# Performance work log

Measured on AMD Instinct MI355X. Metric: run time of the kernel, lower is better.

## Reference

```python
import jax, jax.numpy as jnp
import numpy as np

EPS = 0.001   # EPSILON2
T1 = 1.0
T2 = 100.0
DISC = 16     # number of discrete features
B, F, K1, K2 = 524288, 16, 16, 8


def _enforce(v):
    # Enforced autograd fn: forward = max(v, EPS), backward = identity (STE)
    return v + jax.lax.stop_gradient(jnp.maximum(v, EPS) - v)


def _soft_bin(cont, interval, i_min):
    """cont: [B,F]; interval: [F,K]; i_min: [F]. Vectorized over features/bins.
    Returns (STE one-hot out [B, F*K], kmeans_loss scalar)."""
    # bin centers = i_min + running cumsum of (enforced) gaps -> [F,K]
    centers = i_min[:, None] + jnp.cumsum(_enforce(interval), axis=1)
    d = (cont[:, :, None] - centers[None, :, :]) ** 2          # [B,F,K]
    s1 = jax.nn.softmax(-T1 * d, axis=-1)                      # kmeans softmax
    kmeans_loss = jnp.sum(jnp.mean(jnp.sum(d * s1, axis=-1), axis=0))
    s2 = jax.nn.softmax(-T2 * d, axis=-1)                      # sharp softmax
    oh = jax.nn.one_hot(jnp.argmax(s2, axis=-1), d.shape[-1], dtype=s2.dtype)
    out = s2 + jax.lax.stop_gradient(oh - s2)                  # STE one-hot
    return out.reshape(cont.shape[0], -1), kmeans_loss


def setup_inputs() -> dict:
    key = jax.random.key(0)
    k1, k2, k3 = jax.random.split(key, 3)
    x = jax.random.uniform(k1, (B, DISC + F), dtype=jnp.float32)
    interval = jax.random.uniform(k2, (F, K1), dtype=jnp.float32,
                                  minval=0.01, maxval=0.12)
    interval2 = jax.random.uniform(k3, (F, K2), dtype=jnp.float32,
                                   minval=0.02, maxval=0.2)
    i_min = jnp.zeros((F,), dtype=jnp.float32)
    return {"x": x, "interval": interval, "interval2": interval2, "i_min": i_min}


def reference(x, interval, interval2, i_min):
    x_disc, cont = x[:, :DISC], x[:, DISC:]
    out1, loss1 = _soft_bin(cont, interval, i_min)
    out2, loss2 = _soft_bin(cont, interval2, i_min)
    total_out = jnp.concatenate([x_disc, out1, out2], axis=1)  # [B, DISC+F*(K1+K2)]
    return total_out, loss1 + loss2
```

## Files before the change

### kernel.cpp

```cpp
#include <hip/hip_runtime.h>


constexpr int kB      = 524288;
constexpr int kF      = 16;
constexpr int kK1     = 16;
constexpr int kK2     = 8;
constexpr int kRowIn  = 32;
constexpr int kRowOut = 400;
constexpr float kEps  = 0.001f;
constexpr int kTPB    = 256;
constexpr int kGrid   = kB / kTPB;
constexpr int kC4     = kRowOut / 4;
constexpr int kXStride = 33;

template <int K>
__device__ __forceinline__ int soft_argmax_loss(const float* __restrict__ dd,
                                                double& lacc)
{
#pragma clang fp contract(off)
    float se = 0.f, sde = 0.f;
#pragma unroll
    for (int k = 0; k < K; ++k) {
        float e = __expf(-dd[k]);
        se += e; sde += dd[k] * e;
    }
    lacc += (double)(sde / se);

    float z[K];
#pragma unroll
    for (int k = 0; k < K; ++k) z[k] = -100.0f * dd[k];
    float m = z[0]; int kmax = 0;
#pragma unroll
    for (int k = 1; k < K; ++k) {
        if (z[k] > m) { m = z[k]; kmax = k; }
    }

    bool cand = false;
#pragma unroll
    for (int k = 0; k < K; ++k)
        cand |= (k < kmax) & (z[k] >= m - 2.4e-7f);
    if (cand) {
        float e2[K]; float ss = 0.f;
        for (int k = 0; k < K; ++k) { e2[k] = expf(z[k] - m); ss += e2[k]; }
        int km = 0; float pmax = e2[0] / ss;
        for (int k = 1; k < K; ++k) {
            float p = e2[k] / ss;
            if (p > pmax) { pmax = p; km = k; }
        }
        kmax = km;
    }
    return kmax;
}

__global__ __launch_bounds__(kTPB) void binlayer_main(
    const float* __restrict__ x,
    const float* __restrict__ interval,
    const float* __restrict__ interval2,
    const float* __restrict__ i_min,
    float* __restrict__ out,
    double* __restrict__ partial)
{
#pragma clang fp contract(off)
    __shared__ float sC1[kF][kK1];
    __shared__ float sC2[kF][kK2];
    __shared__ float sX[kTPB * kXStride];
    __shared__ unsigned char sIdx[kTPB * kF];
    __shared__ double sL[kTPB / 64];

    const int tid = threadIdx.x;

    if (tid < kF) {
        const float base = i_min[tid];
        float run = 0.f;
        for (int k = 0; k < kK1; ++k) {
            run += fmaxf(interval[tid * kK1 + k], kEps);
            sC1[tid][k] = base + run;
        }
        run = 0.f;
        for (int k = 0; k < kK2; ++k) {
            run += fmaxf(interval2[tid * kK2 + k], kEps);
            sC2[tid][k] = base + run;
        }
    }

    const long long rowBase = (long long)blockIdx.x * kTPB;

    const float4* __restrict__ xin4 = (const float4*)(x + rowBase * kRowIn);
#pragma unroll
    for (int i = 0; i < (kTPB * kRowIn / 4) / kTPB; ++i) {
        int flat = i * kTPB + tid;
        float4 v = xin4[flat];
        int r = flat >> 3, c4 = flat & 7;
        float* p = &sX[r * kXStride + c4 * 4];
        p[0] = v.x; p[1] = v.y; p[2] = v.z; p[3] = v.w;
    }
    __syncthreads();

    double lacc = 0.0;
    const float* __restrict__ myc = &sX[tid * kXStride + 16];

#pragma unroll 1
    for (int f = 0; f < kF; ++f) {
        const float c = myc[f];

        float dd1[kK1];
#pragma unroll
        for (int k = 0; k < kK1; ++k) { float t = c - sC1[f][k]; dd1[k] = t * t; }
        int k1 = soft_argmax_loss<kK1>(dd1, lacc);

        float dd2[kK2];
#pragma unroll
        for (int k = 0; k < kK2; ++k) { float t = c - sC2[f][k]; dd2[k] = t * t; }
        int k2 = soft_argmax_loss<kK2>(dd2, lacc);

        sIdx[tid * kF + f] = (unsigned char)(k1 | (k2 << 4));
    }

#pragma unroll
    for (int off = 32; off > 0; off >>= 1) lacc += __shfl_down(lacc, off);
    if ((tid & 63) == 0) sL[tid >> 6] = lacc;

    __syncthreads();

    if (tid == 0) partial[blockIdx.x] = sL[0] + sL[1] + sL[2] + sL[3];

    float4* __restrict__ o4 = (float4*)(out + rowBase * kRowOut);
#pragma unroll 1
    for (int i = 0; i < kC4; ++i) {
        unsigned idx = (unsigned)(i * kTPB + tid);
        unsigned r = idx / 100u;
        unsigned c = idx - r * 100u;
        float4 o;
        if (c < 4u) {
            const float* p = &sX[r * kXStride + c * 4u];
            o.x = p[0]; o.y = p[1]; o.z = p[2]; o.w = p[3];
        } else if (c < 68u) {
            unsigned u = c - 4u, f = u >> 2, q = (u & 3u) * 4u;
            unsigned k = sIdx[r * kF + f] & 15u;
            o.x = (k == q + 0u) ? 1.f : 0.f;
            o.y = (k == q + 1u) ? 1.f : 0.f;
            o.z = (k == q + 2u) ? 1.f : 0.f;
            o.w = (k == q + 3u) ? 1.f : 0.f;
        } else {
            unsigned u = c - 68u, f = u >> 1, q = (u & 1u) * 4u;
            unsigned k = (unsigned)(sIdx[r * kF + f]) >> 4;
            o.x = (k == q + 0u) ? 1.f : 0.f;
            o.y = (k == q + 1u) ? 1.f : 0.f;
            o.z = (k == q + 2u) ? 1.f : 0.f;
            o.w = (k == q + 3u) ? 1.f : 0.f;
        }
        o4[idx] = o;
    }
}

__global__ __launch_bounds__(256) void binlayer_finalize(
    const double* __restrict__ partial,
    float* __restrict__ out)
{
    __shared__ double sL[4];
    const int tid = threadIdx.x;
    double s = 0.0;
#pragma unroll
    for (int i = 0; i < kGrid / 256; ++i)
        s += partial[i * 256 + tid];
#pragma unroll
    for (int off = 32; off > 0; off >>= 1) s += __shfl_down(s, off);
    if ((tid & 63) == 0) sL[tid >> 6] = s;
    __syncthreads();
    if (tid == 0)
        out[(long long)kB * kRowOut] =
            (float)((sL[0] + sL[1] + sL[2] + sL[3]) * (1.0 / (double)kB));
}

extern "C" void kernel_launch(void* const* d_in, const int* in_sizes, int n_in,
                              void* d_out, int out_size, void* d_ws, size_t ws_size,
                              hipStream_t stream)
{
    const float* x    = (const float*)d_in[0];
    const float* itv1 = (const float*)d_in[1];
    const float* itv2 = (const float*)d_in[2];
    const float* imin = (const float*)d_in[3];
    float* out = (float*)d_out;
    double* partial = (double*)d_ws;

    binlayer_main<<<kGrid, kTPB, 0, stream>>>(x, itv1, itv2, imin, out, partial);
    binlayer_finalize<<<1, 256, 0, stream>>>(partial, out);
}
```

Measured before the change: 892.4 us.

## Make each wave own its rows to drop block barriers; use nontemporal output stores

Each 64-lane wave now loads, processes and writes only its own 64 rows, so the block-wide barriers after the input load and before the output phase become per-wave LDS waitcnts. When the workspace is large enough, partial loss sums are written per wave, which removes the last barrier, and the finalize kernel loops over a variable count. Output stores use nontemporal hints to limit cache pollution from the large write-only stream. One block barrier is added after the centers setup. The per-wave output writes are less contiguous across the block, and the finalize kernel reads four times as many partials.

```diff
diff --git a/kernel.cpp b/kernel.cpp
--- a/kernel.cpp
+++ b/kernel.cpp
@@ -12,6 +12,9 @@
 constexpr int kGrid   = kB / kTPB;
 constexpr int kC4     = kRowOut / 4;
 constexpr int kXStride = 33;
+constexpr int kWPB    = kTPB / 64;
+
+typedef float f32x4 __attribute__((ext_vector_type(4)));
 
 template <int K>
 __device__ __forceinline__ int soft_argmax_loss(const float* __restrict__ dd,
@@ -58,16 +61,19 @@
     const float* __restrict__ interval2,
     const float* __restrict__ i_min,
     float* __restrict__ out,
-    double* __restrict__ partial)
+    double* __restrict__ partial,
+    int perwave)
 {
 #pragma clang fp contract(off)
     __shared__ float sC1[kF][kK1];
     __shared__ float sC2[kF][kK2];
     __shared__ float sX[kTPB * kXStride];
     __shared__ unsigned char sIdx[kTPB * kF];
-    __shared__ double sL[kTPB / 64];
+    __shared__ double sL[kWPB];
 
     const int tid = threadIdx.x;
+    const int w   = tid >> 6;
+    const int l   = tid & 63;
 
     if (tid < kF) {
         const float base = i_min[tid];
@@ -82,19 +88,21 @@
             sC2[tid][k] = base + run;
         }
     }
+    __syncthreads();
 
     const long long rowBase = (long long)blockIdx.x * kTPB;
-
-    const float4* __restrict__ xin4 = (const float4*)(x + rowBase * kRowIn);
-#pragma unroll
-    for (int i = 0; i < (kTPB * kRowIn / 4) / kTPB; ++i) {
-        int flat = i * kTPB + tid;
-        float4 v = xin4[flat];
-        int r = flat >> 3, c4 = flat & 7;
+    const int R0 = w * 64;
+
+    const f32x4* __restrict__ xin4 = (const f32x4*)(x + (rowBase + R0) * kRowIn);
+#pragma unroll
+    for (int i = 0; i < 8; ++i) {
+        int flat = i * 64 + l;
+        f32x4 v = xin4[flat];
+        int r = R0 + (flat >> 3), c4 = flat & 7;
         float* p = &sX[r * kXStride + c4 * 4];
         p[0] = v.x; p[1] = v.y; p[2] = v.z; p[3] = v.w;
     }
-    __syncthreads();
+    asm volatile("s_waitcnt lgkmcnt(0)" ::: "memory");
 
     double lacc = 0.0;
     const float* __restrict__ myc = &sX[tid * kXStride + 16];
@@ -115,54 +123,58 @@
 
         sIdx[tid * kF + f] = (unsigned char)(k1 | (k2 << 4));
     }
+    asm volatile("s_waitcnt lgkmcnt(0)" ::: "memory");
 
 #pragma unroll
     for (int off = 32; off > 0; off >>= 1) lacc += __shfl_down(lacc, off);
-    if ((tid & 63) == 0) sL[tid >> 6] = lacc;
-
-    __syncthreads();
-
-    if (tid == 0) partial[blockIdx.x] = sL[0] + sL[1] + sL[2] + sL[3];
-
-    float4* __restrict__ o4 = (float4*)(out + rowBase * kRowOut);
+    if (perwave) {
+        if (l == 0) partial[(long long)blockIdx.x * kWPB + w] = lacc;
+    } else {
+        if (l == 0) sL[w] = lacc;
+        __syncthreads();
+        if (tid == 0) partial[blockIdx.x] = sL[0] + sL[1] + sL[2] + sL[3];
+    }
+
+    f32x4* __restrict__ o4 = (f32x4*)(out + (rowBase + R0) * kRowOut);
 #pragma unroll 1
     for (int i = 0; i < kC4; ++i) {
-        unsigned idx = (unsigned)(i * kTPB + tid);
+        unsigned idx = (unsigned)(i * 64 + l);
         unsigned r = idx / 100u;
         unsigned c = idx - r * 100u;
-        float4 o;
+        unsigned rr = (unsigned)R0 + r;
+        f32x4 o;
         if (c < 4u) {
-            const float* p = &sX[r * kXStride + c * 4u];
+            const float* p = &sX[rr * kXStride + c * 4u];
             o.x = p[0]; o.y = p[1]; o.z = p[2]; o.w = p[3];
         } else if (c < 68u) {
             unsigned u = c - 4u, f = u >> 2, q = (u & 3u) * 4u;
-            unsigned k = sIdx[r * kF + f] & 15u;
+            unsigned k = sIdx[rr * kF + f] & 15u;
             o.x = (k == q + 0u) ? 1.f : 0.f;
             o.y = (k == q + 1u) ? 1.f : 0.f;
             o.z = (k == q + 2u) ? 1.f : 0.f;
             o.w = (k == q + 3u) ? 1.f : 0.f;
         } else {
             unsigned u = c - 68u, f = u >> 1, q = (u & 1u) * 4u;
-            unsigned k = (unsigned)(sIdx[r * kF + f]) >> 4;
+            unsigned k = (unsigned)(sIdx[rr * kF + f]) >> 4;
             o.x = (k == q + 0u) ? 1.f : 0.f;
             o.y = (k == q + 1u) ? 1.f : 0.f;
             o.z = (k == q + 2u) ? 1.f : 0.f;
             o.w = (k == q + 3u) ? 1.f : 0.f;
         }
-        o4[idx] = o;
+        __builtin_nontemporal_store(o, &o4[idx]);
     }
 }
 
 __global__ __launch_bounds__(256) void binlayer_finalize(
     const double* __restrict__ partial,
-    float* __restrict__ out)
+    float* __restrict__ out,
+    int n)
 {
     __shared__ double sL[4];
     const int tid = threadIdx.x;
     double s = 0.0;
-#pragma unroll
-    for (int i = 0; i < kGrid / 256; ++i)
-        s += partial[i * 256 + tid];
+    for (int i = tid; i < n; i += 256)
+        s += partial[i];
 #pragma unroll
     for (int off = 32; off > 0; off >>= 1) s += __shfl_down(s, off);
     if ((tid & 63) == 0) sL[tid >> 6] = s;
@@ -183,6 +195,9 @@
     float* out = (float*)d_out;
     double* partial = (double*)d_ws;
 
-    binlayer_main<<<kGrid, kTPB, 0, stream>>>(x, itv1, itv2, imin, out, partial);
-    binlayer_finalize<<<1, 256, 0, stream>>>(partial, out);
-}
+    const int perwave = (ws_size >= (size_t)kGrid * kWPB * sizeof(double)) ? 1 : 0;
+    const int nPartial = perwave ? kGrid * kWPB : kGrid;
+
+    binlayer_main<<<kGrid, kTPB, 0, stream>>>(x, itv1, itv2, imin, out, partial, perwave);
+    binlayer_finalize<<<1, 256, 0, stream>>>(partial, out, nPartial);
+}
```

Result: slower. 911.5 us (+2.1%).

## Split fused kernel into compute-indices and expand-output kernels via workspace

Applied to the files above, without the earlier changes.

Splits the single fused kernel into two. The first computes the packed bin indices and per-warp loss partials directly from global memory, without staging x in shared memory. The second reads those indices and x and writes the 400-float output rows in a fully coalesced grid-strided pattern. The aim is to drop the large shared-memory footprint, raising occupancy, and to let the memory-bound output write run as its own streaming kernel. In exchange it adds an 8 MB index round trip through global memory and an extra launch, and the new path only runs if the workspace is large enough.

```diff
diff --git a/kernel.cpp b/kernel.cpp
--- a/kernel.cpp
+++ b/kernel.cpp
@@ -12,6 +12,14 @@
 constexpr int kGrid   = kB / kTPB;
 constexpr int kC4     = kRowOut / 4;
 constexpr int kXStride = 33;
+constexpr int kWPB    = kTPB / 64;
+
+constexpr size_t kIdxBytes = (size_t)kB * kF;
+constexpr size_t kPartOff  = kIdxBytes;
+constexpr size_t kWsNeed   = kIdxBytes + (size_t)kGrid * kWPB * sizeof(double);
+
+typedef float f32x4 __attribute__((ext_vector_type(4)));
+typedef unsigned long long u64x2 __attribute__((ext_vector_type(2)));
 
 template <int K>
 __device__ __forceinline__ int soft_argmax_loss(const float* __restrict__ dd,
@@ -50,6 +58,108 @@
         kmax = km;
     }
     return kmax;
+}
+
+__device__ __forceinline__ f32x4 onehot4(unsigned k, unsigned q)
+{
+    f32x4 o;
+    o.x = (k == q + 0u) ? 1.f : 0.f;
+    o.y = (k == q + 1u) ? 1.f : 0.f;
+    o.z = (k == q + 2u) ? 1.f : 0.f;
+    o.w = (k == q + 3u) ? 1.f : 0.f;
+    return o;
+}
+
+__global__ __launch_bounds__(kTPB) void bin_compute(
+    const float* __restrict__ x,
+    const float* __restrict__ interval,
+    const float* __restrict__ interval2,
+    const float* __restrict__ i_min,
+    unsigned long long* __restrict__ idxbuf,
+    double* __restrict__ partial)
+{
+#pragma clang fp contract(off)
+    __shared__ float sC1[kF][kK1];
+    __shared__ float sC2[kF][kK2];
+
+    const int tid = threadIdx.x;
+    const int w   = tid >> 6;
+    const int l   = tid & 63;
+
+    if (tid < kF) {
+        const float base = i_min[tid];
+        float run = 0.f;
+        for (int k = 0; k < kK1; ++k) {
+            run += fmaxf(interval[tid * kK1 + k], kEps);
+            sC1[tid][k] = base + run;
+        }
+        run = 0.f;
+        for (int k = 0; k < kK2; ++k) {
+            run += fmaxf(interval2[tid * kK2 + k], kEps);
+            sC2[tid][k] = base + run;
+        }
+    }
+    __syncthreads();
+
+    const long long row = (long long)blockIdx.x * kTPB + tid;
+    const float* __restrict__ xr = x + row * kRowIn + 16;
+
+    double lacc = 0.0;
+    unsigned long long lo = 0ull, hi = 0ull;
+
+#pragma unroll 1
+    for (int f = 0; f < kF; ++f) {
+        const float c = xr[f];
+
+        float dd1[kK1];
+#pragma unroll
+        for (int k = 0; k < kK1; ++k) { float t = c - sC1[f][k]; dd1[k] = t * t; }
+        int k1 = soft_argmax_loss<kK1>(dd1, lacc);
+
+        float dd2[kK2];
+#pragma unroll
+        for (int k = 0; k < kK2; ++k) { float t = c - sC2[f][k]; dd2[k] = t * t; }
+        int k2 = soft_argmax_loss<kK2>(dd2, lacc);
+
+        const unsigned long long byte = (unsigned long long)(k1 | (k2 << 4));
+        if (f < 8) lo |= byte << (8 * f);
+        else       hi |= byte << (8 * (f - 8));
+    }
+
+    u64x2 pk; pk.x = lo; pk.y = hi;
+    *reinterpret_cast<u64x2*>(&idxbuf[row * 2]) = pk;
+
+#pragma unroll
+    for (int off = 32; off > 0; off >>= 1) lacc += __shfl_down(lacc, off);
+    if (l == 0) partial[(long long)blockIdx.x * kWPB + w] = lacc;
+}
+
+__global__ __launch_bounds__(kTPB) void bin_expand(
+    const float* __restrict__ x,
+    const unsigned char* __restrict__ ib,
+    float* __restrict__ out)
+{
+    const unsigned t0 = blockIdx.x * kTPB + threadIdx.x;
+    f32x4* __restrict__ o4 = (f32x4*)out;
+
+#pragma unroll 1
+    for (int s = 0; s < kC4; ++s) {
+        const unsigned chunk = (unsigned)s * (unsigned)kB + t0;
+        const unsigned r = chunk / 100u;
+        const unsigned c = chunk - r * 100u;
+        f32x4 o;
+        if (c < 4u) {
+            o = *reinterpret_cast<const f32x4*>(x + (size_t)r * kRowIn + c * 4u);
+        } else {
+            const unsigned u = c - 4u;
+            unsigned f, q, k;
+            if (u < 64u) { f = u >> 2; q = (u & 3u) * 4u; k = ib[r * 16u + f] & 15u; }
+            else { const unsigned uu = u - 64u; f = uu >> 1; q = (uu & 1u) * 4u;
+                   k = (unsigned)(ib[r * 16u + f]) >> 4; }
+            o = onehot4(k, q);
+        }
+        o4[chunk] = o;
+    }
 }
 
 __global__ __launch_bounds__(kTPB) void binlayer_main(
@@ -155,14 +265,14 @@
 
 __global__ __launch_bounds__(256) void binlayer_finalize(
     const double* __restrict__ partial,
-    float* __restrict__ out)
+    float* __restrict__ out,
+    int n)
 {
     __shared__ double sL[4];
     const int tid = threadIdx.x;
     double s = 0.0;
-#pragma unroll
-    for (int i = 0; i < kGrid / 256; ++i)
-        s += partial[i * 256 + tid];
+    for (int i = tid; i < n; i += 256)
+        s += partial[i];
 #pragma unroll
     for (int off = 32; off > 0; off >>= 1) s += __shfl_down(s, off);
     if ((tid & 63) == 0) sL[tid >> 6] = s;
@@ -181,8 +291,16 @@
     const float* itv2 = (const float*)d_in[2];
     const float* imin = (const float*)d_in[3];
     float* out = (float*)d_out;
-    double* partial = (double*)d_ws;
-
-    binlayer_main<<<kGrid, kTPB, 0, stream>>>(x, itv1, itv2, imin, out, partial);
-    binlayer_finalize<<<1, 256, 0, stream>>>(partial, out);
-}
+
+    if (ws_size >= kWsNeed) {
+        unsigned long long* idxbuf = (unsigned long long*)d_ws;
+        double* partial = (double*)((char*)d_ws + kPartOff);
+        bin_compute<<<kGrid, kTPB, 0, stream>>>(x, itv1, itv2, imin, idxbuf, partial);
+        bin_expand<<<kGrid, kTPB, 0, stream>>>(x, (const unsigned char*)d_ws, out);
+        binlayer_finalize<<<1, 256, 0, stream>>>(partial, out, kGrid * kWPB);
+    } else {
+        double* partial = (double*)d_ws;
+        binlayer_main<<<kGrid, kTPB, 0, stream>>>(x, itv1, itv2, imin, out, partial);
+        binlayer_finalize<<<1, 256, 0, stream>>>(partial, out, kGrid);
+    }
+}
```

Measured after the change: 1.087 ms. 21.8% more time.
